# Kernel tuning notes

Measured on AMD Instinct MI355X. Metric: run time of the kernel, lower is better.

Reference implementation:

```python
import jax, jax.numpy as jnp
import numpy as np

N_SPECIES = 4
NUM_MODELS = 8
LAYER_DIMS = [384, 160, 128, 96, 1]
CELU_ALPHA = 0.1
N_ATOMS = 50000  # divisible by N_SPECIES -> balanced routing


def setup_inputs() -> dict:
    key = jax.random.key(0)
    ks = jax.random.split(key, 2 + 2 * (len(LAYER_DIMS) - 1))
    # Balanced species assignment: exactly N_ATOMS/N_SPECIES atoms per species,
    # randomly permuted (mirrors a real molecule's scattered per-species atoms
    # while keeping per-species group sizes static for jit).
    base = jnp.tile(jnp.arange(N_SPECIES, dtype=jnp.int64), N_ATOMS // N_SPECIES)
    species = jax.random.permutation(ks[0], base)[None, :]  # [1, N_ATOMS]
    aev = jax.random.normal(ks[1], (1, N_ATOMS, LAYER_DIMS[0]), dtype=jnp.float32)
    inp = {"species": species, "aev": aev}
    # Fused ensemble params per species: W [S, M, in, out], b [S, M, 1, out]
    for li in range(len(LAYER_DIMS) - 1):
        fin, fout = LAYER_DIMS[li], LAYER_DIMS[li + 1]
        scale = 1.0 / np.sqrt(fin)
        inp[f"W{li+1}"] = jax.random.uniform(
            ks[2 + 2 * li], (N_SPECIES, NUM_MODELS, fin, fout),
            dtype=jnp.float32, minval=-scale, maxval=scale)
        inp[f"b{li+1}"] = jax.random.uniform(
            ks[3 + 2 * li], (N_SPECIES, NUM_MODELS, 1, fout),
            dtype=jnp.float32, minval=-scale, maxval=scale)
    return inp


def _ensemble_mlp(x, W1, b1, W2, b2, W3, b3, W4, b4):
    # x: [S, n, F] routed atoms per species; W: [S, M, fin, fout]; b: [S, M, 1, fout]
    celu = lambda h: jax.nn.celu(h, alpha=CELU_ALPHA)
    h = celu(jnp.einsum('snf,smfo->smno', x, W1) + b1)   # [S, M, n, 160]
    h = celu(jnp.einsum('smnf,smfo->smno', h, W2) + b2)  # [S, M, n, 128]
    h = celu(jnp.einsum('smnf,smfo->smno', h, W3) + b3)  # [S, M, n, 96]
    h = jnp.einsum('smnf,smfo->smno', h, W4) + b4        # [S, M, n, 1]
    return h.mean(axis=1)                                 # mean over models -> [S, n, 1]


def reference(species, aev, W1, b1, W2, b2, W3, b3, W4, b4):
    n_atoms = species.shape[1]
    n_per = n_atoms // N_SPECIES
    # species-routed gather: stable argsort groups atoms by species; counts are
    # static (balanced) so reshape into [S, n_per] groups (== per-species index_select)
    order = jnp.argsort(species.reshape(-1), stable=True)
    x = aev.reshape(n_atoms, -1)[order].reshape(N_SPECIES, n_per, -1)
    atom_e = _ensemble_mlp(x, W1, b1, W2, b2, W3, b3, W4, b4)  # [S, n_per, 1]
    mol_energies = jnp.sum(atom_e).reshape(1)  # scatter-sum over all atoms/species
    return mol_energies
```

## Files before the change

kernel.cpp:

```cpp
#include <hip/hip_runtime.h>


#define NSP 4
#define NMODELS 8
#define MSPLIT 2
#define MPB (NMODELS / MSPLIT)
#define NATOMS 50000
#define NPER (NATOMS / NSP)
#define NPAD 12544
#define D0 384
#define D1 160
#define D2 128
#define D3 96
#define NRBLK ((NATOMS + 255) / 256)
#define ABLK 128
#define BPS ((NPER + ABLK - 1) / ABLK)
#define FRAGS_SM 184
#define CHUNKS_M 23
#define TOT_CHUNKS (MPB * CHUNKS_M)

typedef float f32x4 __attribute__((ext_vector_type(4)));
typedef __bf16 bf16x8 __attribute__((ext_vector_type(8)));

#define MFMA16(a, b, c) __builtin_amdgcn_mfma_f32_16x16x32_bf16((a), (b), (c), 0, 0, 0)

#define PALL_BYTES ((size_t)NSP * NMODELS * FRAGS_SM * 1024)
#define PBIAS_OFF PALL_BYTES
#define PBIAS_BYTES ((size_t)NSP * NMODELS * 512 * 2)
#define ORDER_OFF (PBIAS_OFF + PBIAS_BYTES)
#define BCNT_OFF (ORDER_OFF + (size_t)NATOMS * 4)
#define BPFX_OFF (BCNT_OFF + (size_t)NRBLK * NSP * 4)
#define BASE_OFF (BPFX_OFF + (size_t)NRBLK * NSP * 4)
#define AEVB_OFF (BASE_OFF + 1024)
#define AEVB_BYTES ((size_t)NSP * NPAD * D0 * 2)

static __device__ __forceinline__ unsigned short bfbits(float f) {
  __bf16 h = (__bf16)f;
  return __builtin_bit_cast(unsigned short, h);
}

static __device__ __forceinline__ float celu01(float x) {
  return fmaxf(x, 0.f) + 0.1f * fminf(0.f, __expf(x * 10.f) - 1.f);
}

static __device__ __forceinline__ void gload16(const void* g, void* l) {
  __builtin_amdgcn_global_load_lds(
      (const __attribute__((address_space(1))) unsigned int*)g,
      (__attribute__((address_space(3))) unsigned int*)l, 16, 0, 0);
}

__global__ __launch_bounds__(256) void count_kernel(const int* __restrict__ species,
                                                    int* __restrict__ bcnt) {
  __shared__ int cnt[NSP];
  int t = threadIdx.x;
  if (t < NSP) cnt[t] = 0;
  __syncthreads();
  int i = blockIdx.x * 256 + t;
  if (i < NATOMS) atomicAdd(&cnt[species[i]], 1);
  __syncthreads();
  if (t < NSP) bcnt[blockIdx.x * NSP + t] = cnt[t];
}

__global__ __launch_bounds__(256) void scan_kernel(const int* __restrict__ bcnt,
                                                   int* __restrict__ bpfx,
                                                   int* __restrict__ base) {
  int w = threadIdx.x >> 6;
  int lane = threadIdx.x & 63;
  __shared__ int totals[NSP];
  int carry = 0;
  for (int c = 0; c < (NRBLK + 63) / 64; ++c) {
    int idx = c * 64 + lane;
    int v = (idx < NRBLK) ? bcnt[idx * NSP + w] : 0;
    int incl = v;
    for (int off = 1; off < 64; off <<= 1) {
      int tv = __shfl_up(incl, off);
      if (lane >= off) incl += tv;
    }
    if (idx < NRBLK) bpfx[idx * NSP + w] = carry + incl - v;
    carry += __shfl(incl, 63);
  }
  if (lane == 0) totals[w] = carry;
  __syncthreads();
  if (threadIdx.x == 0) {
    int run = 0;
    for (int s = 0; s < NSP; ++s) { base[s] = run; run += totals[s]; }
  }
}

__global__ __launch_bounds__(256) void route_kernel(const int* __restrict__ species,
                                                    const int* __restrict__ bpfx,
                                                    const int* __restrict__ base,
                                                    int* __restrict__ order) {
  __shared__ int sp[256];
  int t = threadIdx.x;
  int i = blockIdx.x * 256 + t;
  sp[t] = (i < NATOMS) ? species[i] : -1;
  __syncthreads();
  if (i < NATOMS) {
    int s = sp[t];
    int rank = 0;
    for (int j = 0; j < t; ++j) rank += (sp[j] == s) ? 1 : 0;
    order[base[s] + bpfx[blockIdx.x * NSP + s] + rank] = i;
  }
}

__global__ __launch_bounds__(256) void aev_pack(const float* __restrict__ aev,
                                                const int* __restrict__ order,
                                                unsigned short* __restrict__ aevb) {
  int tid = blockIdx.x * 256 + threadIdx.x;
  const int perRow = D0 / 8;
  int row = tid / perRow;
  int seg = tid - row * perRow;
  if (row >= NSP * NPAD) return;
  int s = row / NPAD;
  int slot = row - s * NPAD;
  unsigned short o[8];
  if (slot < NPER) {
    int src = order[s * NPER + slot];
    const float4* q = (const float4*)(aev + (size_t)src * D0 + seg * 8);
    float4 v0 = q[0], v1 = q[1];
    o[0] = bfbits(v0.x); o[1] = bfbits(v0.y); o[2] = bfbits(v0.z); o[3] = bfbits(v0.w);
    o[4] = bfbits(v1.x); o[5] = bfbits(v1.y); o[6] = bfbits(v1.z); o[7] = bfbits(v1.w);
  } else {
#pragma unroll
    for (int e = 0; e < 8; ++e) o[e] = 0;
  }
  *(int4*)(aevb + (size_t)row * D0 + seg * 8) = *(const int4*)o;
}

__global__ __launch_bounds__(256) void pack_kernel(const float* __restrict__ W,
                                                   unsigned* __restrict__ dst,
                                                   int K, int N, int NT, int fragBase,
                                                   int total) {
  int tid = blockIdx.x * 256 + threadIdx.x;
  if (tid >= total) return;
  int per_sm = K * N / 2;
  int smi = tid / per_sm;
  int rem = tid - smi * per_sm;
  int frag = rem >> 8;
  int wi = rem & 255;
  int l = wi >> 2, d = wi & 3;
  int kf = frag / NT;
  int nt = frag - kf * NT;
  int k = kf * 32 + ((l >> 4) << 3) + 2 * d;
  int n = nt * 16 + (l & 15);
  const float* p = W + ((size_t)smi * K + k) * N + n;
  unsigned lo = bfbits(p[0]);
  unsigned hi = bfbits(p[N]);
  dst[((size_t)smi * FRAGS_SM + fragBase + frag) * 256 + wi] = lo | (hi << 16);
}

__global__ __launch_bounds__(256) void param_pack(const float* __restrict__ b1,
                                                  const float* __restrict__ b2,
                                                  const float* __restrict__ b3,
                                                  const float* __restrict__ W4,
                                                  const float* __restrict__ b4,
                                                  unsigned short* __restrict__ dst) {
  int i = blockIdx.x * 256 + threadIdx.x;
  if (i >= NSP * NMODELS * 512) return;
  int smi = i >> 9, o = i & 511;
  unsigned short v = 0;
  if (o < 160) v = bfbits(b1[smi * 160 + o]);
  else if (o < 288) v = bfbits(b2[smi * 128 + (o - 160)]);
  else if (o < 384) v = bfbits(b3[smi * 96 + (o - 288)]);
  else if (o < 480) v = bfbits(W4[smi * 96 + (o - 384)]);
  else if (o < 482) {
    unsigned u = __builtin_bit_cast(unsigned, b4[smi]);
    v = (unsigned short)((o == 480) ? (u & 0xffffu) : (u >> 16));
  }
  dst[i] = v;
}

#define CHUNK_HDR()                                                      \
  do {                                                                   \
    asm volatile("s_waitcnt vmcnt(2)" ::: "memory");                     \
    __builtin_amdgcn_s_barrier();                                        \
    const char* _src = wsrc + (size_t)tn * 8192;                         \
    char* _d = (char*)stage + wb_off + w * 2048;                         \
    gload16(_src, _d);                                                   \
    gload16(_src + 1024, _d + 1024);                                     \
    tn = (tn + 1 == TOT_CHUNKS) ? 0 : (tn + 1);                          \
    wb_off = (wb_off == 16384u) ? 0u : (wb_off + 8192u);                 \
  } while (0)

#define CHUNK_END() rb_off = (rb_off == 16384u) ? 0u : (rb_off + 8192u)

__global__ __launch_bounds__(256, 2) void mlp_kernel(
    const unsigned short* __restrict__ aevb,
    const unsigned short* __restrict__ pAll, const unsigned short* __restrict__ pPar,
    float* __restrict__ out) {
  __shared__ alignas(16) unsigned short stage[3][4096];
  __shared__ alignas(16) __bf16 hbuf[4][32][168];
  __shared__ alignas(16) unsigned short hpar[MPB * 512];

  const int nwg = NSP * BPS * MSPLIT;
  const int cpx = nwg / 8;
  const int blk = (blockIdx.x % 8) * cpx + blockIdx.x / 8;
  const int s = blk / (BPS * MSPLIT);
  const int rem = blk - s * (BPS * MSPLIT);
  const int mh = rem / BPS;
  const int sb = rem - mh * BPS;
  const int tid = threadIdx.x;
  const int w = tid >> 6;
  const int l = tid & 63;
  const int l15 = l & 15;
  const int l4 = l >> 4;

  {
    const int4* src = (const int4*)(pPar + ((size_t)(s * NMODELS + mh * MPB)) * 512);
    ((int4*)hpar)[tid] = src[tid];
  }

  const size_t smBase = (size_t)(s * NMODELS + mh * MPB) * FRAGS_SM;
  const char* wsrc = (const char*)pAll + smBase * 1024 + (size_t)w * 2048 + (size_t)l * 16;

  bf16x8 a1[2][12];
#pragma unroll
  for (int mt = 0; mt < 2; ++mt) {
    int row = s * NPAD + sb * ABLK + w * 32 + mt * 16 + l15;
    const bf16x8* rp = (const bf16x8*)(aevb + (size_t)row * D0 + l4 * 8);
#pragma unroll
    for (int kf = 0; kf < 12; ++kf) a1[mt][kf] = rp[kf * 4];
  }

  const __bf16* hb = (const __bf16*)hpar;
  float acc4[2][4] = {{0.f, 0.f, 0.f, 0.f}, {0.f, 0.f, 0.f, 0.f}};
  float bbacc = 0.f;

  __syncthreads();

  int tn = 2;
  unsigned rb_off = 0, wb_off = 16384u;
  {
    char* d0 = (char*)stage + w * 2048;
    gload16(wsrc, d0);
    gload16(wsrc + 1024, d0 + 1024);
    char* d1 = (char*)stage + 8192 + w * 2048;
    gload16(wsrc + 8192, d1);
    gload16(wsrc + 8192 + 1024, d1 + 1024);
  }

#pragma unroll 1
  for (int m = 0; m < MPB; ++m) {
    f32x4 C[2][10];

#pragma unroll
    for (int mt = 0; mt < 2; ++mt)
#pragma unroll
      for (int nt = 0; nt < 10; ++nt) {
        f32x4 z; z[0] = z[1] = z[2] = z[3] = 0.f; C[mt][nt] = z;
      }
#pragma unroll
    for (int c = 0; c < 15; ++c) {
      CHUNK_HDR();
      const bf16x8* sbuf = (const bf16x8*)((const char*)stage + rb_off);
#pragma unroll
      for (int j = 0; j < 8; ++j) {
        const int f = c * 8 + j;
        bf16x8 b = sbuf[j * 64 + l];
        C[0][f % 10] = MFMA16(a1[0][f / 10], b, C[0][f % 10]);
        C[1][f % 10] = MFMA16(a1[1][f / 10], b, C[1][f % 10]);
      }
      CHUNK_END();
    }
#pragma unroll
    for (int nt = 0; nt < 10; ++nt) {
      float bias = (float)hb[m * 512 + nt * 16 + l15];
#pragma unroll
      for (int mt = 0; mt < 2; ++mt)
#pragma unroll
        for (int r = 0; r < 4; ++r)
          hbuf[w][mt * 16 + l4 * 4 + r][nt * 16 + l15] = (__bf16)celu01(C[mt][nt][r] + bias);
    }

    bf16x8 a2[2][5];
#pragma unroll
    for (int mt = 0; mt < 2; ++mt)
#pragma unroll
      for (int kf = 0; kf < 5; ++kf)
        a2[mt][kf] = *(const bf16x8*)&hbuf[w][mt * 16 + l15][kf * 32 + l4 * 8];

#pragma unroll
    for (int mt = 0; mt < 2; ++mt)
#pragma unroll
      for (int nt = 0; nt < 8; ++nt) {
        f32x4 z; z[0] = z[1] = z[2] = z[3] = 0.f; C[mt][nt] = z;
      }
#pragma unroll
    for (int lc = 0; lc < 5; ++lc) {
      CHUNK_HDR();
      const bf16x8* sbuf = (const bf16x8*)((const char*)stage + rb_off);
#pragma unroll
      for (int j = 0; j < 8; ++j) {
        bf16x8 b = sbuf[j * 64 + l];
        C[0][j] = MFMA16(a2[0][lc], b, C[0][j]);
        C[1][j] = MFMA16(a2[1][lc], b, C[1][j]);
      }
      CHUNK_END();
    }
#pragma unroll
    for (int nt = 0; nt < 8; ++nt) {
      float bias = (float)hb[m * 512 + 160 + nt * 16 + l15];
#pragma unroll
      for (int mt = 0; mt < 2; ++mt)
#pragma unroll
        for (int r = 0; r < 4; ++r)
          hbuf[w][mt * 16 + l4 * 4 + r][nt * 16 + l15] = (__bf16)celu01(C[mt][nt][r] + bias);
    }

    bf16x8 a3[2][4];
#pragma unroll
    for (int mt = 0; mt < 2; ++mt)
#pragma unroll
      for (int kf = 0; kf < 4; ++kf)
        a3[mt][kf] = *(const bf16x8*)&hbuf[w][mt * 16 + l15][kf * 32 + l4 * 8];

#pragma unroll
    for (int mt = 0; mt < 2; ++mt)
#pragma unroll
      for (int nt = 0; nt < 6; ++nt) {
        f32x4 z; z[0] = z[1] = z[2] = z[3] = 0.f; C[mt][nt] = z;
      }
#pragma unroll
    for (int lc = 0; lc < 3; ++lc) {
      CHUNK_HDR();
      const bf16x8* sbuf = (const bf16x8*)((const char*)stage + rb_off);
#pragma unroll
      for (int j = 0; j < 8; ++j) {
        const int f = lc * 8 + j;
        bf16x8 b = sbuf[j * 64 + l];
        C[0][f % 6] = MFMA16(a3[0][f / 6], b, C[0][f % 6]);
        C[1][f % 6] = MFMA16(a3[1][f / 6], b, C[1][f % 6]);
      }
      CHUNK_END();
    }

    float e[2][4] = {{0.f, 0.f, 0.f, 0.f}, {0.f, 0.f, 0.f, 0.f}};
#pragma unroll
    for (int nt = 0; nt < 6; ++nt) {
      float b3v = (float)hb[m * 512 + 288 + nt * 16 + l15];
      float w4v = (float)hb[m * 512 + 384 + nt * 16 + l15];
#pragma unroll
      for (int mt = 0; mt < 2; ++mt)
#pragma unroll
        for (int r = 0; r < 4; ++r)
          e[mt][r] += celu01(C[mt][nt][r] + b3v) * w4v;
    }
#pragma unroll
    for (int mt = 0; mt < 2; ++mt)
#pragma unroll
      for (int r = 0; r < 4; ++r) acc4[mt][r] += e[mt][r];
    bbacc += ((const float*)hpar)[m * 256 + 240];
  }

  asm volatile("s_waitcnt vmcnt(0)" ::: "memory");

  float tot = 0.f;
#pragma unroll
  for (int mt = 0; mt < 2; ++mt)
#pragma unroll
    for (int r = 0; r < 4; ++r) {
      float v = acc4[mt][r];
      v += __shfl_xor(v, 1);
      v += __shfl_xor(v, 2);
      v += __shfl_xor(v, 4);
      v += __shfl_xor(v, 8);
      int slot = sb * ABLK + w * 32 + mt * 16 + l4 * 4 + r;
      if (l15 == 0 && slot < NPER) tot += v + bbacc;
    }
  tot *= (1.f / NMODELS);
#pragma unroll
  for (int off = 1; off < 64; off <<= 1) tot += __shfl_xor(tot, off);
  if (l == 0) atomicAdd(out, tot);
}

extern "C" void kernel_launch(void* const* d_in, const int* in_sizes, int n_in,
                              void* d_out, int out_size, void* d_ws, size_t ws_size,
                              hipStream_t stream) {
  (void)in_sizes; (void)n_in; (void)out_size; (void)ws_size;
  const int* species = (const int*)d_in[0];
  const float* aev = (const float*)d_in[1];
  const float* W1 = (const float*)d_in[2];
  const float* b1 = (const float*)d_in[3];
  const float* W2 = (const float*)d_in[4];
  const float* b2 = (const float*)d_in[5];
  const float* W3 = (const float*)d_in[6];
  const float* b3 = (const float*)d_in[7];
  const float* W4 = (const float*)d_in[8];
  const float* b4 = (const float*)d_in[9];
  float* out = (float*)d_out;
  char* ws = (char*)d_ws;

  unsigned short* pAll = (unsigned short*)ws;
  unsigned short* pPar = (unsigned short*)(ws + PBIAS_OFF);
  int* order = (int*)(ws + ORDER_OFF);
  int* bcnt = (int*)(ws + BCNT_OFF);
  int* bpfx = (int*)(ws + BPFX_OFF);
  int* base = (int*)(ws + BASE_OFF);
  unsigned short* aevb = (unsigned short*)(ws + AEVB_OFF);

  hipMemsetAsync(d_out, 0, sizeof(float), stream);

  count_kernel<<<NRBLK, 256, 0, stream>>>(species, bcnt);
  scan_kernel<<<1, 256, 0, stream>>>(bcnt, bpfx, base);
  route_kernel<<<NRBLK, 256, 0, stream>>>(species, bpfx, base, order);

  {
    int total = NSP * NPAD * (D0 / 8);
    aev_pack<<<total / 256, 256, 0, stream>>>(aev, order, aevb);
  }
  {
    int total = NSP * NMODELS * D0 * D1 / 2;
    pack_kernel<<<(total + 255) / 256, 256, 0, stream>>>(W1, (unsigned*)pAll, D0, D1, D1 / 16, 0, total);
  }
  {
    int total = NSP * NMODELS * D1 * D2 / 2;
    pack_kernel<<<(total + 255) / 256, 256, 0, stream>>>(W2, (unsigned*)pAll, D1, D2, D2 / 16, 120, total);
  }
  {
    int total = NSP * NMODELS * D2 * D3 / 2;
    pack_kernel<<<(total + 255) / 256, 256, 0, stream>>>(W3, (unsigned*)pAll, D2, D3, D3 / 16, 160, total);
  }
  {
    int total = NSP * NMODELS * 512;
    param_pack<<<(total + 255) / 256, 256, 0, stream>>>(b1, b2, b3, W4, b4, pPar);
  }

  mlp_kernel<<<NSP * BPS * MSPLIT, 256, 0, stream>>>(aevb, pAll, pPar, out);
}
```

Before: 218.6 us.

## Use 8 waves per block with 16 atom rows each instead of 4x32

Doubles the block size to 512 threads so each wave processes one 16-row M tile instead of two. This halves per-thread accumulator and A-fragment registers, and launch bounds now request 4 blocks per CU. Each wave loads one 1KB slice of the shared weight chunk, and the vmcnt wait drops to match. The intent is more waves resident per CU to hide latency. The cost is that each weight fragment read from LDS now feeds one MFMA instead of two, lowering reuse and doubling LDS read traffic per FLOP.

Result: slower. 250.6 us (+14.6%).

```diff
diff --git a/kernel.cpp b/kernel.cpp
--- a/kernel.cpp
+++ b/kernel.cpp
@@ -173,24 +173,21 @@
 
 #define CHUNK_HDR()                                                      \
   do {                                                                   \
-    asm volatile("s_waitcnt vmcnt(2)" ::: "memory");                     \
+    asm volatile("s_waitcnt vmcnt(1)" ::: "memory");                     \
     __builtin_amdgcn_s_barrier();                                        \
-    const char* _src = wsrc + (size_t)tn * 8192;                         \
-    char* _d = (char*)stage + wb_off + w * 2048;                         \
-    gload16(_src, _d);                                                   \
-    gload16(_src + 1024, _d + 1024);                                     \
+    gload16(wsrc + (size_t)tn * 8192, (char*)stage + wb_off + w * 1024); \
     tn = (tn + 1 == TOT_CHUNKS) ? 0 : (tn + 1);                          \
     wb_off = (wb_off == 16384u) ? 0u : (wb_off + 8192u);                 \
   } while (0)
 
 #define CHUNK_END() rb_off = (rb_off == 16384u) ? 0u : (rb_off + 8192u)
 
-__global__ __launch_bounds__(256, 2) void mlp_kernel(
+__global__ __launch_bounds__(512, 4) void mlp_kernel(
     const unsigned short* __restrict__ aevb,
     const unsigned short* __restrict__ pAll, const unsigned short* __restrict__ pPar,
     float* __restrict__ out) {
   __shared__ alignas(16) unsigned short stage[3][4096];
-  __shared__ alignas(16) __bf16 hbuf[4][32][168];
+  __shared__ alignas(16) __bf16 hbuf[8][16][168];
   __shared__ alignas(16) unsigned short hpar[MPB * 512];
 
   const int nwg = NSP * BPS * MSPLIT;
@@ -206,50 +203,41 @@
   const int l15 = l & 15;
   const int l4 = l >> 4;
 
-  {
+  if (tid < 256) {
     const int4* src = (const int4*)(pPar + ((size_t)(s * NMODELS + mh * MPB)) * 512);
     ((int4*)hpar)[tid] = src[tid];
   }
 
   const size_t smBase = (size_t)(s * NMODELS + mh * MPB) * FRAGS_SM;
-  const char* wsrc = (const char*)pAll + smBase * 1024 + (size_t)w * 2048 + (size_t)l * 16;
-
-  bf16x8 a1[2][12];
-#pragma unroll
-  for (int mt = 0; mt < 2; ++mt) {
-    int row = s * NPAD + sb * ABLK + w * 32 + mt * 16 + l15;
+  const char* wsrc = (const char*)pAll + smBase * 1024 + (size_t)w * 1024 + (size_t)l * 16;
+
+  bf16x8 a1[12];
+  {
+    int row = s * NPAD + sb * ABLK + w * 16 + l15;
     const bf16x8* rp = (const bf16x8*)(aevb + (size_t)row * D0 + l4 * 8);
 #pragma unroll
-    for (int kf = 0; kf < 12; ++kf) a1[mt][kf] = rp[kf * 4];
+    for (int kf = 0; kf < 12; ++kf) a1[kf] = rp[kf * 4];
   }
 
   const __bf16* hb = (const __bf16*)hpar;
-  float acc4[2][4] = {{0.f, 0.f, 0.f, 0.f}, {0.f, 0.f, 0.f, 0.f}};
+  float acc4[4] = {0.f, 0.f, 0.f, 0.f};
   float bbacc = 0.f;
 
   __syncthreads();
 
   int tn = 2;
   unsigned rb_off = 0, wb_off = 16384u;
-  {
-    char* d0 = (char*)stage + w * 2048;
-    gload16(wsrc, d0);
-    gload16(wsrc + 1024, d0 + 1024);
-    char* d1 = (char*)stage + 8192 + w * 2048;
-    gload16(wsrc + 8192, d1);
-    gload16(wsrc + 8192 + 1024, d1 + 1024);
-  }
+  gload16(wsrc, (char*)stage + w * 1024);
+  gload16(wsrc + 8192, (char*)stage + 8192 + w * 1024);
 
 #pragma unroll 1
   for (int m = 0; m < MPB; ++m) {
-    f32x4 C[2][10];
-
-#pragma unroll
-    for (int mt = 0; mt < 2; ++mt)
-#pragma unroll
-      for (int nt = 0; nt < 10; ++nt) {
-        f32x4 z; z[0] = z[1] = z[2] = z[3] = 0.f; C[mt][nt] = z;
-      }
+    f32x4 C[10];
+
+#pragma unroll
+    for (int nt = 0; nt < 10; ++nt) {
+      f32x4 z; z[0] = z[1] = z[2] = z[3] = 0.f; C[nt] = z;
+    }
 #pragma unroll
     for (int c = 0; c < 15; ++c) {
       CHUNK_HDR();
@@ -258,8 +246,7 @@
       for (int j = 0; j < 8; ++j) {
         const int f = c * 8 + j;
         bf16x8 b = sbuf[j * 64 + l];
-        C[0][f % 10] = MFMA16(a1[0][f / 10], b, C[0][f % 10]);
-        C[1][f % 10] = MFMA16(a1[1][f / 10], b, C[1][f % 10]);
+        C[f % 10] = MFMA16(a1[f / 10], b, C[f % 10]);
       }
       CHUNK_END();
     }
@@ -267,25 +254,19 @@
     for (int nt = 0; nt < 10; ++nt) {
       float bias = (float)hb[m * 512 + nt * 16 + l15];
 #pragma unroll
-      for (int mt = 0; mt < 2; ++mt)
-#pragma unroll
-        for (int r = 0; r < 4; ++r)
-          hbuf[w][mt * 16 + l4 * 4 + r][nt * 16 + l15] = (__bf16)celu01(C[mt][nt][r] + bias);
-    }
-
-    bf16x8 a2[2][5];
-#pragma unroll
-    for (int mt = 0; mt < 2; ++mt)
-#pragma unroll
-      for (int kf = 0; kf < 5; ++kf)
-        a2[mt][kf] = *(const bf16x8*)&hbuf[w][mt * 16 + l15][kf * 32 + l4 * 8];
-
-#pragma unroll
-    for (int mt = 0; mt < 2; ++mt)
-#pragma unroll
-      for (int nt = 0; nt < 8; ++nt) {
-        f32x4 z; z[0] = z[1] = z[2] = z[3] = 0.f; C[mt][nt] = z;
-      }
+      for (int r = 0; r < 4; ++r)
+        hbuf[w][l4 * 4 + r][nt * 16 + l15] = (__bf16)celu01(C[nt][r] + bias);
+    }
+
+    bf16x8 a2[5];
+#pragma unroll
+    for (int kf = 0; kf < 5; ++kf)
+      a2[kf] = *(const bf16x8*)&hbuf[w][l15][kf * 32 + l4 * 8];
+
+#pragma unroll
+    for (int nt = 0; nt < 8; ++nt) {
+      f32x4 z; z[0] = z[1] = z[2] = z[3] = 0.f; C[nt] = z;
+    }
 #pragma unroll
     for (int lc = 0; lc < 5; ++lc) {
       CHUNK_HDR();
@@ -293,8 +274,7 @@
 #pragma unroll
       for (int j = 0; j < 8; ++j) {
         bf16x8 b = sbuf[j * 64 + l];
-        C[0][j] = MFMA16(a2[0][lc], b, C[0][j]);
-        C[1][j] = MFMA16(a2[1][lc], b, C[1][j]);
+        C[j] = MFMA16(a2[lc], b, C[j]);
       }
       CHUNK_END();
     }
@@ -302,25 +282,19 @@
     for (int nt = 0; nt < 8; ++nt) {
       float bias = (float)hb[m * 512 + 160 + nt * 16 + l15];
 #pragma unroll
-      for (int mt = 0; mt < 2; ++mt)
-#pragma unroll
-        for (int r = 0; r < 4; ++r)
-          hbuf[w][mt * 16 + l4 * 4 + r][nt * 16 + l15] = (__bf16)celu01(C[mt][nt][r] + bias);
-    }
-
-    bf16x8 a3[2][4];
-#pragma unroll
-    for (int mt = 0; mt < 2; ++mt)
-#pragma unroll
-      for (int kf = 0; kf < 4; ++kf)
-        a3[mt][kf] = *(const bf16x8*)&hbuf[w][mt * 16 + l15][kf * 32 + l4 * 8];
-
-#pragma unroll
-    for (int mt = 0; mt < 2; ++mt)
-#pragma unroll
-      for (int nt = 0; nt < 6; ++nt) {
-        f32x4 z; z[0] = z[1] = z[2] = z[3] = 0.f; C[mt][nt] = z;
-      }
+      for (int r = 0; r < 4; ++r)
+        hbuf[w][l4 * 4 + r][nt * 16 + l15] = (__bf16)celu01(C[nt][r] + bias);
+    }
+
+    bf16x8 a3[4];
+#pragma unroll
+    for (int kf = 0; kf < 4; ++kf)
+      a3[kf] = *(const bf16x8*)&hbuf[w][l15][kf * 32 + l4 * 8];
+
+#pragma unroll
+    for (int nt = 0; nt < 6; ++nt) {
+      f32x4 z; z[0] = z[1] = z[2] = z[3] = 0.f; C[nt] = z;
+    }
 #pragma unroll
     for (int lc = 0; lc < 3; ++lc) {
       CHUNK_HDR();
@@ -329,27 +303,22 @@
       for (int j = 0; j < 8; ++j) {
         const int f = lc * 8 + j;
         bf16x8 b = sbuf[j * 64 + l];
-        C[0][f % 6] = MFMA16(a3[0][f / 6], b, C[0][f % 6]);
-        C[1][f % 6] = MFMA16(a3[1][f / 6], b, C[1][f % 6]);
+        C[f % 6] = MFMA16(a3[f / 6], b, C[f % 6]);
       }
       CHUNK_END();
     }
 
-    float e[2][4] = {{0.f, 0.f, 0.f, 0.f}, {0.f, 0.f, 0.f, 0.f}};
+    float e[4] = {0.f, 0.f, 0.f, 0.f};
 #pragma unroll
     for (int nt = 0; nt < 6; ++nt) {
       float b3v = (float)hb[m * 512 + 288 + nt * 16 + l15];
       float w4v = (float)hb[m * 512 + 384 + nt * 16 + l15];
 #pragma unroll
-      for (int mt = 0; mt < 2; ++mt)
-#pragma unroll
-        for (int r = 0; r < 4; ++r)
-          e[mt][r] += celu01(C[mt][nt][r] + b3v) * w4v;
-    }
-#pragma unroll
-    for (int mt = 0; mt < 2; ++mt)
-#pragma unroll
-      for (int r = 0; r < 4; ++r) acc4[mt][r] += e[mt][r];
+      for (int r = 0; r < 4; ++r)
+        e[r] += celu01(C[nt][r] + b3v) * w4v;
+    }
+#pragma unroll
+    for (int r = 0; r < 4; ++r) acc4[r] += e[r];
     bbacc += ((const float*)hpar)[m * 256 + 240];
   }
 
@@ -357,17 +326,15 @@
 
   float tot = 0.f;
 #pragma unroll
-  for (int mt = 0; mt < 2; ++mt)
-#pragma unroll
-    for (int r = 0; r < 4; ++r) {
-      float v = acc4[mt][r];
-      v += __shfl_xor(v, 1);
-      v += __shfl_xor(v, 2);
-      v += __shfl_xor(v, 4);
-      v += __shfl_xor(v, 8);
-      int slot = sb * ABLK + w * 32 + mt * 16 + l4 * 4 + r;
-      if (l15 == 0 && slot < NPER) tot += v + bbacc;
-    }
+  for (int r = 0; r < 4; ++r) {
+    float v = acc4[r];
+    v += __shfl_xor(v, 1);
+    v += __shfl_xor(v, 2);
+    v += __shfl_xor(v, 4);
+    v += __shfl_xor(v, 8);
+    int slot = sb * ABLK + w * 16 + l4 * 4 + r;
+    if (l15 == 0 && slot < NPER) tot += v + bbacc;
+  }
   tot *= (1.f / NMODELS);
 #pragma unroll
   for (int off = 1; off < 64; off <<= 1) tot += __shfl_xor(tot, off);
@@ -426,5 +393,5 @@
     param_pack<<<(total + 255) / 256, 256, 0, stream>>>(b1, b2, b3, W4, b4, pPar);
   }
 
-  mlp_kernel<<<NSP * BPS * MSPLIT, 256, 0, stream>>>(aevb, pAll, pPar, out);
-}
+  mlp_kernel<<<NSP * BPS * MSPLIT, 512, 0, stream>>>(aevb, pAll, pPar, out);
+}
```
